# Performance work log

Hardware: AMD Instinct MI355X
Metric: run time of the kernel (lower is better)

Reference implementation:

```python
import jax, jax.numpy as jnp
import numpy as np

H = W = 1536
DT = 0.02
FAST_DT, SLOW_DT = 1.0, 0.2
EPS_FAST, EPS_SLOW = 0.06, 0.02
F2S, S2F = 0.04, 0.02


def setup_inputs() -> dict:
    key = jax.random.key(0)
    k1, k2, k3 = jax.random.split(key, 3)
    phi = jax.random.normal(k1, (1, 10, H, W), jnp.float32)
    sensory_map = jax.random.normal(k2, (1, 1, H, W), jnp.float32)
    gamma = jnp.array([0.2, 0.15, 0.1, 0.18, 0.12, 0.13, 0.14, 0.16, 0.11, 0.1], jnp.float32)
    alpha = jnp.array([0.3, 0.25, 0.22, 0.18, 0.2, 0.15, 0.19, 0.24, 0.17, 0.16], jnp.float32)
    mix_w = jax.random.normal(k3, (10, 10), jnp.float32) * 0.1  # 1x1 conv weight, no bias
    return {"phi": phi, "sensory_map": sensory_map, "gamma": gamma, "alpha": alpha, "mix_w": mix_w}


def _lap(x):
    # periodic 5-point Laplacian via rolls on the last two (spatial) dims
    return (jnp.roll(x, 1, -2) + jnp.roll(x, -1, -2)
            + jnp.roll(x, 1, -1) + jnp.roll(x, -1, -1) - 4.0 * x)


def _step(phi, sensory_map, gamma, alpha, mix_w):
    lap = _lap(phi)
    bilap = _lap(lap)
    g, a, p = gamma, alpha, phi
    ch = [
        -g[0] * lap[:, 0] - a[0] * p[:, 0] ** 3 + 0.12 * bilap[:, 0],
        -g[1] * lap[:, 1] + 0.15 * jnp.sin(p[:, 1]) + 0.08 * p[:, 1] ** 3,
        -g[2] * lap[:, 2] + 0.2 * p[:, 2] * (1.0 - p[:, 2] ** 2),
        -g[3] * lap[:, 3] - 0.03 * p[:, 3] ** 5 + 0.08 * bilap[:, 3],
        -g[4] * lap[:, 4] + 0.12 * p[:, 4] * jnp.log(jnp.abs(p[:, 4]) + 1e-6) + 0.02 * bilap[:, 4],
        -g[5] * lap[:, 5] + 0.08 * p[:, 5] ** 3 - 0.02 * p[:, 5] ** 5,
        -g[6] * lap[:, 6] + 0.06 * p[:, 6] ** 4 - 0.04 * p[:, 6],
        -g[7] * lap[:, 7] + 0.08 * jnp.sinh(jnp.clip(p[:, 7], -2.0, 2.0)),
        -g[8] * lap[:, 8] + 0.05 * p[:, 8] ** 2 - 0.08 * p[:, 8],
        -g[9] * lap[:, 9] + 0.02 * p[:, 9] ** 6 - 0.04 * p[:, 9] ** 3 + 0.01 * bilap[:, 9],
    ]
    dphi = jnp.stack(ch, axis=1)                                 # [1,10,H,W]
    coupling = jnp.einsum('oc,bchw->bohw', mix_w, phi)            # 1x1 conv, no bias
    fast_mean = phi[:, :5].mean(axis=1, keepdims=True)            # [1,1,H,W]
    slow_mean = phi[:, 5:].mean(axis=1, keepdims=True)
    sd = sensory_map[:, 0]                                        # [1,H,W]
    dphi_f = dphi[:, :5] + EPS_FAST * coupling[:, :5] + S2F * slow_mean
    dphi_s = dphi[:, 5:] + EPS_SLOW * coupling[:, 5:] + F2S * fast_mean
    dphi_f = dphi_f.at[:, 0].add(0.2 * sd).at[:, 4].add(0.08 * jnp.abs(sd))
    dphi_s = dphi_s.at[:, 4].add(0.05 * sd)                       # global channel 9
    phi_next = jnp.concatenate([phi[:, :5] + DT * FAST_DT * dphi_f,
                                phi[:, 5:] + DT * SLOW_DT * dphi_s], axis=1)
    return jnp.clip(phi_next, -4.0, 4.0)


def reference(phi, sensory_map, gamma, alpha, mix_w):
    phi_next = _step(phi, sensory_map, gamma, alpha, mix_w)
    phi1_mean = phi_next[:, 0].mean(axis=(1, 2))
    phi5_mean = phi_next[:, 4].mean(axis=(1, 2))
    field_means = phi_next.mean(axis=(2, 3))
    return phi_next, phi1_mean, phi5_mean, field_means
```

## Files before the change

kernel.cpp:

```cpp
#include <hip/hip_runtime.h>
#include <math.h>

#define HH 1536
#define WW 1536
#define HWSZ (HH*WW)
#define NT 384
#define NBLK (HH*2)


__device__ __forceinline__ float2 LD2(const float* __restrict__ p, int row, int idx) {
    return reinterpret_cast<const float2*>(p + row)[idx];
}

__global__ __launch_bounds__(NT) void step_kernel(
    const float* __restrict__ phi,
    const float* __restrict__ sensory,
    const float* __restrict__ gamma,
    const float* __restrict__ alpha,
    const float* __restrict__ mixw,
    float* __restrict__ out,
    float* __restrict__ sums)
{
    __shared__ float s_mix[100];
    __shared__ float s_g[10];
    __shared__ float s_a0;
    __shared__ float s_red[6][10];

    const int tid = threadIdx.x;
    if (tid < 100) s_mix[tid] = mixw[tid];
    if (tid < 10)  s_g[tid]   = gamma[tid];
    if (tid == 0)  s_a0       = alpha[0];
    __syncthreads();

    const int blk = blockIdx.x;
    const int nb   = (blk & 7) * 384 + (blk >> 3);
    const int y    = nb >> 1;
    const int half = nb & 1;

    const int col = half * 384 + tid;
    const int x0  = col * 2;

    const int ym1 = (y == 0)      ? HH - 1     : y - 1;
    const int yp1 = (y == HH - 1) ? 0          : y + 1;
    const int ym2 = (y < 2)       ? y + HH - 2 : y - 2;
    const int yp2 = (y >= HH - 2) ? y - HH + 2 : y + 2;

    const int r0  = y   * WW;
    const int rm1 = ym1 * WW;
    const int rp1 = yp1 * WW;
    const int rm2 = ym2 * WW;
    const int rp2 = yp2 * WW;

    const int xl1 = (x0 == 0)      ? WW - 1 : x0 - 1;
    const int xl2 = (x0 == 0)      ? WW - 2 : x0 - 2;
    const int xr1 = (x0 + 2 == WW) ? 0      : x0 + 2;
    const int xr2 = (x0 + 2 == WW) ? 1      : x0 + 3;

    float pv[10][2];
    float dv[10][2];

    #pragma unroll
    for (int c = 0; c < 10; ++c) {
        const float* pc = phi + (size_t)c * HWSZ;
        const float2 cm = LD2(pc, r0,  col);
        const float2 nn = LD2(pc, rm1, col);
        const float2 ss = LD2(pc, rp1, col);
        const float wl1 = pc[r0 + xl1];
        const float wr1 = pc[r0 + xr1];

        float lap[2];
        lap[0] = nn.x + ss.x + wl1  + cm.y - 4.0f * cm.x;
        lap[1] = nn.y + ss.y + cm.x + wr1  - 4.0f * cm.y;

        float bl[2] = {0.f, 0.f};
        if (c == 0 || c == 3 || c == 4 || c == 9) {
            const float2 t2n = LD2(pc, rm2, col);
            const float2 t2s = LD2(pc, rp2, col);
            const float wl2 = pc[r0  + xl2];
            const float wr2 = pc[r0  + xr2];
            const float nwl = pc[rm1 + xl1];
            const float ner = pc[rm1 + xr1];
            const float swl = pc[rp1 + xl1];
            const float ser = pc[rp1 + xr1];
            bl[0] = 20.0f*cm.x - 8.0f*(nn.x + ss.x + wl1  + cm.y)
                  + 2.0f*(nwl  + nn.y + swl + ss.y) + (t2n.x + t2s.x + wl2 + wr1);
            bl[1] = 20.0f*cm.y - 8.0f*(nn.y + ss.y + cm.x + wr1)
                  + 2.0f*(nn.x + ner  + ss.x + ser) + (t2n.y + t2s.y + wl1 + wr2);
        }

        pv[c][0] = cm.x; pv[c][1] = cm.y;

        #pragma unroll
        for (int k = 0; k < 2; ++k) {
            const float pp = pv[c][k];
            const float lv = lap[k];
            const float bv = bl[k];
            float dd;
            switch (c) {
            case 0: dd = -s_g[0]*lv - s_a0*pp*pp*pp + 0.12f*bv; break;
            case 1: dd = -s_g[1]*lv + 0.15f*sinf(pp) + 0.08f*pp*pp*pp; break;
            case 2: dd = -s_g[2]*lv + 0.2f*pp*(1.0f - pp*pp); break;
            case 3: { const float p2 = pp*pp;
                      dd = -s_g[3]*lv - 0.03f*p2*p2*pp + 0.08f*bv; } break;
            case 4: dd = -s_g[4]*lv + 0.12f*pp*logf(fabsf(pp) + 1e-6f) + 0.02f*bv; break;
            case 5: { const float p2 = pp*pp;
                      dd = -s_g[5]*lv + 0.08f*p2*pp - 0.02f*p2*p2*pp; } break;
            case 6: { const float p2 = pp*pp;
                      dd = -s_g[6]*lv + 0.06f*p2*p2 - 0.04f*pp; } break;
            case 7: { const float pc7 = fminf(fmaxf(pp, -2.0f), 2.0f);
                      dd = -s_g[7]*lv + 0.08f*sinhf(pc7); } break;
            case 8: dd = -s_g[8]*lv + 0.05f*pp*pp - 0.08f*pp; break;
            default: { const float p3 = pp*pp*pp;
                       dd = -s_g[9]*lv + 0.02f*p3*p3 - 0.04f*p3 + 0.01f*bv; } break;
            }
            dv[c][k] = dd;
        }
    }

    float fmv[2], smv[2], sdk[2];
    {
        const float2 sd2 = LD2(sensory, r0, col);
        sdk[0] = sd2.x; sdk[1] = sd2.y;
        #pragma unroll
        for (int k = 0; k < 2; ++k) {
            fmv[k] = (pv[0][k] + pv[1][k] + pv[2][k] + pv[3][k] + pv[4][k]) * 0.2f;
            smv[k] = (pv[5][k] + pv[6][k] + pv[7][k] + pv[8][k] + pv[9][k]) * 0.2f;
        }
    }

    const int lane = tid & 63;
    const int wave = tid >> 6;

    #pragma unroll
    for (int o = 0; o < 10; ++o) {
        float pn[2];
        #pragma unroll
        for (int k = 0; k < 2; ++k) {
            float cp = 0.0f;
            #pragma unroll
            for (int c = 0; c < 10; ++c) cp = fmaf(s_mix[o*10 + c], pv[c][k], cp);
            float dd = dv[o][k];
            if (o < 5) {
                dd += 0.06f * cp + 0.02f * smv[k];
                if (o == 0) dd += 0.2f  * sdk[k];
                if (o == 4) dd += 0.08f * fabsf(sdk[k]);
                pn[k] = pv[o][k] + 0.02f * dd;
            } else {
                dd += 0.02f * cp + 0.04f * fmv[k];
                if (o == 9) dd += 0.05f * sdk[k];
                pn[k] = pv[o][k] + 0.004f * dd;
            }
            pn[k] = fminf(fmaxf(pn[k], -4.0f), 4.0f);
        }
        float2 o2; o2.x = pn[0]; o2.y = pn[1];
        reinterpret_cast<float2*>(out + (size_t)o * HWSZ + r0)[col] = o2;

        float s = pn[0] + pn[1];
        #pragma unroll
        for (int off = 32; off > 0; off >>= 1) s += __shfl_down(s, off, 64);
        if (lane == 0) s_red[wave][o] = s;
    }

    __syncthreads();
    if (tid < 10) {
        float v = 0.0f;
        #pragma unroll
        for (int w = 0; w < 6; ++w) v += s_red[w][tid];
        atomicAdd(&sums[tid], v);
    }
}

__global__ void finalize_kernel(const float* __restrict__ sums,
                                float* __restrict__ out)
{
    const int t = threadIdx.x;
    const float inv = 1.0f / (float)HWSZ;
    const size_t base = (size_t)10 * HWSZ;
    if (t == 0) out[base]     = sums[0] * inv;
    if (t == 1) out[base + 1] = sums[4] * inv;
    if (t >= 2 && t < 12) out[base + 2 + (t - 2)] = sums[t - 2] * inv;
}

extern "C" void kernel_launch(void* const* d_in, const int* in_sizes, int n_in,
                              void* d_out, int out_size, void* d_ws, size_t ws_size,
                              hipStream_t stream) {
    const float* phi     = (const float*)d_in[0];
    const float* sensory = (const float*)d_in[1];
    const float* gamma   = (const float*)d_in[2];
    const float* alpha   = (const float*)d_in[3];
    const float* mixw    = (const float*)d_in[4];
    float* out = (float*)d_out;
    float* sums = (float*)d_ws;

    hipMemsetAsync(sums, 0, 10 * sizeof(float), stream);

    step_kernel<<<dim3(NBLK), NT, 0, stream>>>(phi, sensory, gamma, alpha, mixw, out, sums);
    finalize_kernel<<<1, 64, 0, stream>>>(sums, out);
}
```

Before: 267.8 us.

## Compute 1x1 coupling upfront and stream per-channel outputs, use 256-thread blocks

The kernel now makes a first pass over the center values of all 10 channels to build the 1x1-conv coupling terms and the fast/slow means. A second per-channel pass computes the stencil, finishes the update and stores each output channel at once. This removes the pv/dv arrays kept live across all channels, which is meant to lower register pressure, at the cost of loading the center values twice. Block size drops from 384 to 256 threads and each row is split into 3 parts, with the banded block remapping adjusted to match.

```diff
diff --git a/kernel.cpp b/kernel.cpp
--- a/kernel.cpp
+++ b/kernel.cpp
@@ -4,8 +4,9 @@
 #define HH 1536
 #define WW 1536
 #define HWSZ (HH*WW)
-#define NT 384
-#define NBLK (HH*2)
+#define NT 256
+#define NBLK (HH*3)
+#define BAND (NBLK/8)
 
 
 __device__ __forceinline__ float2 LD2(const float* __restrict__ p, int row, int idx) {
@@ -24,7 +25,7 @@
     __shared__ float s_mix[100];
     __shared__ float s_g[10];
     __shared__ float s_a0;
-    __shared__ float s_red[6][10];
+    __shared__ float s_red[4][10];
 
     const int tid = threadIdx.x;
     if (tid < 100) s_mix[tid] = mixw[tid];
@@ -32,12 +33,12 @@
     if (tid == 0)  s_a0       = alpha[0];
     __syncthreads();
 
-    const int blk = blockIdx.x;
-    const int nb   = (blk & 7) * 384 + (blk >> 3);
-    const int y    = nb >> 1;
-    const int half = nb & 1;
-
-    const int col = half * 384 + tid;
+    const int blk  = blockIdx.x;
+    const int nb   = (blk & 7) * BAND + (blk >> 3);
+    const int y    = nb / 3;
+    const int part = nb - y * 3;
+
+    const int col = part * NT + tid;
     const int x0  = col * 2;
 
     const int ym1 = (y == 0)      ? HH - 1     : y - 1;
@@ -56,8 +57,33 @@
     const int xr1 = (x0 + 2 == WW) ? 0      : x0 + 2;
     const int xr2 = (x0 + 2 == WW) ? 1      : x0 + 3;
 
-    float pv[10][2];
-    float dv[10][2];
+    float cp[10][2];
+    #pragma unroll
+    for (int o = 0; o < 10; ++o) { cp[o][0] = 0.0f; cp[o][1] = 0.0f; }
+    float fm0 = 0.f, fm1 = 0.f, sm0 = 0.f, sm1 = 0.f;
+
+    #pragma unroll
+    for (int c = 0; c < 10; ++c) {
+        const float2 v = LD2(phi + (size_t)c * HWSZ, r0, col);
+        #pragma unroll
+        for (int o = 0; o < 10; ++o) {
+            const float m = s_mix[o * 10 + c];
+            cp[o][0] = fmaf(m, v.x, cp[o][0]);
+            cp[o][1] = fmaf(m, v.y, cp[o][1]);
+        }
+        if (c < 5) { fm0 += v.x; fm1 += v.y; }
+        else       { sm0 += v.x; sm1 += v.y; }
+    }
+    fm0 *= 0.2f; fm1 *= 0.2f; sm0 *= 0.2f; sm1 *= 0.2f;
+
+    float sd0, sd1;
+    {
+        const float2 sd2 = LD2(sensory, r0, col);
+        sd0 = sd2.x; sd1 = sd2.y;
+    }
+
+    const int lane = tid & 63;
+    const int wave = tid >> 6;
 
     #pragma unroll
     for (int c = 0; c < 10; ++c) {
@@ -88,11 +114,11 @@
                   + 2.0f*(nn.x + ner  + ss.x + ser) + (t2n.y + t2s.y + wl1 + wr2);
         }
 
-        pv[c][0] = cm.x; pv[c][1] = cm.y;
-
+        const float pvk[2] = {cm.x, cm.y};
+        float pn[2];
         #pragma unroll
         for (int k = 0; k < 2; ++k) {
-            const float pp = pv[c][k];
+            const float pp = pvk[k];
             const float lv = lap[k];
             const float bv = bl[k];
             float dd;
@@ -113,59 +139,35 @@
             default: { const float p3 = pp*pp*pp;
                        dd = -s_g[9]*lv + 0.02f*p3*p3 - 0.04f*p3 + 0.01f*bv; } break;
             }
-            dv[c][k] = dd;
-        }
-    }
-
-    float fmv[2], smv[2], sdk[2];
-    {
-        const float2 sd2 = LD2(sensory, r0, col);
-        sdk[0] = sd2.x; sdk[1] = sd2.y;
-        #pragma unroll
-        for (int k = 0; k < 2; ++k) {
-            fmv[k] = (pv[0][k] + pv[1][k] + pv[2][k] + pv[3][k] + pv[4][k]) * 0.2f;
-            smv[k] = (pv[5][k] + pv[6][k] + pv[7][k] + pv[8][k] + pv[9][k]) * 0.2f;
-        }
-    }
-
-    const int lane = tid & 63;
-    const int wave = tid >> 6;
-
-    #pragma unroll
-    for (int o = 0; o < 10; ++o) {
-        float pn[2];
-        #pragma unroll
-        for (int k = 0; k < 2; ++k) {
-            float cp = 0.0f;
-            #pragma unroll
-            for (int c = 0; c < 10; ++c) cp = fmaf(s_mix[o*10 + c], pv[c][k], cp);
-            float dd = dv[o][k];
-            if (o < 5) {
-                dd += 0.06f * cp + 0.02f * smv[k];
-                if (o == 0) dd += 0.2f  * sdk[k];
-                if (o == 4) dd += 0.08f * fabsf(sdk[k]);
-                pn[k] = pv[o][k] + 0.02f * dd;
+
+            const float sdk = (k == 0) ? sd0 : sd1;
+            if (c < 5) {
+                dd += 0.06f * cp[c][k] + 0.02f * ((k == 0) ? sm0 : sm1);
+                if (c == 0) dd += 0.2f  * sdk;
+                if (c == 4) dd += 0.08f * fabsf(sdk);
+                pn[k] = pp + 0.02f * dd;
             } else {
-                dd += 0.02f * cp + 0.04f * fmv[k];
-                if (o == 9) dd += 0.05f * sdk[k];
-                pn[k] = pv[o][k] + 0.004f * dd;
+                dd += 0.02f * cp[c][k] + 0.04f * ((k == 0) ? fm0 : fm1);
+                if (c == 9) dd += 0.05f * sdk;
+                pn[k] = pp + 0.004f * dd;
             }
             pn[k] = fminf(fmaxf(pn[k], -4.0f), 4.0f);
         }
+
         float2 o2; o2.x = pn[0]; o2.y = pn[1];
-        reinterpret_cast<float2*>(out + (size_t)o * HWSZ + r0)[col] = o2;
+        reinterpret_cast<float2*>(out + (size_t)c * HWSZ + r0)[col] = o2;
 
         float s = pn[0] + pn[1];
         #pragma unroll
         for (int off = 32; off > 0; off >>= 1) s += __shfl_down(s, off, 64);
-        if (lane == 0) s_red[wave][o] = s;
+        if (lane == 0) s_red[wave][c] = s;
     }
 
     __syncthreads();
     if (tid < 10) {
         float v = 0.0f;
         #pragma unroll
-        for (int w = 0; w < 6; ++w) v += s_red[w][tid];
+        for (int w = 0; w < 4; ++w) v += s_red[w][tid];
         atomicAdd(&sums[tid], v);
     }
 }
```

Measured after the change: 242.6 us. 1.1x faster.
